# Kernel tuning notes

Measured on AMD Instinct MI355X. Metric: run time of the kernel, lower is better.

## Reference

```python
import jax, jax.numpy as jnp
import numpy as np

S, D_IN, D_OUT = 4096, 1024, 1024

def setup_inputs() -> dict:
    key = jax.random.key(0)
    kx, kq, kk, kv = jax.random.split(key, 4)
    scale = 0.02
    return {
        "x": jax.random.normal(kx, (S, D_IN), dtype=jnp.float32),
        "W_query": jax.random.normal(kq, (D_IN, D_OUT), dtype=jnp.float32) * scale,
        "W_key": jax.random.normal(kk, (D_IN, D_OUT), dtype=jnp.float32) * scale,
        "W_value": jax.random.normal(kv, (D_IN, D_OUT), dtype=jnp.float32) * scale,
    }

def reference(x, W_query, W_key, W_value):
    # x: [S, d_in]; W_*: [d_in, d_out]
    queries = x @ W_query        # [S, d_out]
    keys = x @ W_key             # [S, d_out]
    values = x @ W_value         # [S, d_out]
    d_k = keys.shape[-1]
    attn_scores = queries @ keys.T            # [S, S]
    attn_weights = jax.nn.softmax(attn_scores / jnp.sqrt(jnp.float32(d_k)), axis=-1)
    context_vec = attn_weights @ values       # [S, d_out]
    return context_vec
```

## Files before the change

kernel.cpp:

```cpp
#include <hip/hip_runtime.h>
#include <hip/hip_bf16.h>

typedef _Float16 f16x8 __attribute__((ext_vector_type(8)));
typedef float f32x4 __attribute__((ext_vector_type(4)));
typedef unsigned short u16;
typedef u16 u16x8 __attribute__((ext_vector_type(8)));

__device__ __forceinline__ u16 f2h_bits(float f) {
    _Float16 h = (_Float16)f;
    return __builtin_bit_cast(u16, h);
}
__device__ __forceinline__ float h2f(u16 b) {
    return (float)__builtin_bit_cast(_Float16, b);
}
__device__ __forceinline__ float ld_as_float(const float* p) { return *p; }
__device__ __forceinline__ float ld_as_float(const u16* p)   { return h2f(*p); }

__device__ __forceinline__ void async_ld16(const void* g, void* l) {
    __builtin_amdgcn_global_load_lds(
        (__attribute__((address_space(1))) void*)(void*)g,
        (__attribute__((address_space(3))) void*)l,
        16, 0, 0);
}

__device__ __forceinline__ void store_val(float* p, float v) { *p = v; }
__device__ __forceinline__ void store_val(u16* p, float v)   { *p = f2h_bits(v); }

template <typename OutT>
__global__ __launch_bounds__(256) void gemm_bt(
    const u16* __restrict__ A, int lda,
    const u16* __restrict__ B, int ldb,
    OutT* __restrict__ C, int ldc,
    int Ksplit, float alpha, size_t c_z_stride)
{
    __shared__ __attribute__((aligned(16))) u16 As[128 * 32];
    __shared__ __attribute__((aligned(16))) u16 Bs[128 * 32];

    const int t    = threadIdx.x;
    const int lane = t & 63;
    const int wave = t >> 6;
    const int wm   = wave & 1;
    const int wn   = wave >> 1;
    const int l16  = lane & 15;
    const int quad = lane >> 4;

    const int bm = blockIdx.y;
    const int bn = blockIdx.x;
    const int kz = blockIdx.z;
    A += (size_t)kz * Ksplit;
    B += (size_t)kz * Ksplit;
    C += (size_t)kz * c_z_stride;

    const int srow = t >> 2;
    const int sseg = (t & 3) ^ ((t >> 3) & 3);
    const int scol = sseg * 8;

    const u16* Ag = A + (size_t)(bm * 128 + srow) * lda + scol;
    const u16* Bg = B + (size_t)(bn * 128 + srow) * ldb + scol;
    const size_t a64 = (size_t)64 * lda;
    const size_t b64 = (size_t)64 * ldb;

    u16* AsD0 = &As[t * 8];
    u16* AsD1 = &As[2048 + t * 8];
    u16* BsD0 = &Bs[t * 8];
    u16* BsD1 = &Bs[2048 + t * 8];

    const int fseg = (quad ^ ((l16 >> 1) & 3)) * 8;
    const u16* Afr = &As[(wm * 64 + l16) * 32 + fseg];
    const u16* Bfr = &Bs[(wn * 64 + l16) * 32 + fseg];

    f32x4 acc[4][4] = {};

    for (int k0 = 0; k0 < Ksplit; k0 += 32) {
        async_ld16(Ag + k0,       AsD0);
        async_ld16(Ag + k0 + a64, AsD1);
        async_ld16(Bg + k0,       BsD0);
        async_ld16(Bg + k0 + b64, BsD1);
        __syncthreads();

        f16x8 af[4], bfv[4];
#pragma unroll
        for (int i = 0; i < 4; i++) af[i]  = *(const f16x8*)(Afr + i * 16 * 32);
#pragma unroll
        for (int i = 0; i < 4; i++) bfv[i] = *(const f16x8*)(Bfr + i * 16 * 32);

#pragma unroll
        for (int mi = 0; mi < 4; mi++)
#pragma unroll
            for (int ni = 0; ni < 4; ni++)
                acc[mi][ni] = __builtin_amdgcn_mfma_f32_16x16x32_f16(
                    af[mi], bfv[ni], acc[mi][ni], 0, 0, 0);

        __syncthreads();
    }

    const int crow = bm * 128 + wm * 64 + quad * 4;
    const int ccol = bn * 128 + wn * 64 + l16;
#pragma unroll
    for (int mi = 0; mi < 4; mi++) {
#pragma unroll
        for (int ni = 0; ni < 4; ni++) {
#pragma unroll
            for (int r = 0; r < 4; r++) {
                float v = acc[mi][ni][r] * alpha;
                store_val(C + (size_t)(crow + mi * 16 + r) * ldc + (ccol + ni * 16), v);
            }
        }
    }
}

__global__ __launch_bounds__(256) void cast_to_f16(
    const float* __restrict__ in, u16* __restrict__ out, int n)
{
    int i = (blockIdx.x * 256 + threadIdx.x) * 4;
    if (i + 3 < n) {
        float4 v = *(const float4*)(in + i);
        ushort4 o;
        o.x = f2h_bits(v.x);
        o.y = f2h_bits(v.y);
        o.z = f2h_bits(v.z);
        o.w = f2h_bits(v.w);
        *(ushort4*)(out + i) = o;
    }
}

template <typename InT>
__global__ __launch_bounds__(256) void transpose_to_f16(
    const InT* __restrict__ in, int ld_in,
    u16* __restrict__ out, int ld_out)
{
    __shared__ float tile[32][33];
    const int bx = blockIdx.x * 32;
    const int by = blockIdx.y * 32;
    const int tx = threadIdx.x, ty = threadIdx.y;
#pragma unroll
    for (int j = 0; j < 4; j++)
        tile[ty + j * 8][tx] = ld_as_float(&in[(size_t)(by + ty + j * 8) * ld_in + bx + tx]);
    __syncthreads();
#pragma unroll
    for (int j = 0; j < 4; j++)
        out[(size_t)(bx + ty + j * 8) * ld_out + by + tx] = f2h_bits(tile[tx][ty + j * 8]);
}

__global__ __launch_bounds__(256) void softmax_rows(u16* __restrict__ S)
{
    const int row = blockIdx.x;
    u16* p = S + (size_t)row * 4096 + threadIdx.x * 16;
    const int t = threadIdx.x;

    u16x8 h0 = *(const u16x8*)p;
    u16x8 h1 = *(const u16x8*)(p + 8);
    float v[16];
    float m = -1e30f;
#pragma unroll
    for (int i = 0; i < 8; i++) { v[i]     = h2f(h0[i]); m = fmaxf(m, v[i]); }
#pragma unroll
    for (int i = 0; i < 8; i++) { v[i + 8] = h2f(h1[i]); m = fmaxf(m, v[i + 8]); }
#pragma unroll
    for (int o = 32; o > 0; o >>= 1) m = fmaxf(m, __shfl_xor(m, o));

    __shared__ float redm[4], reds[4];
    if ((t & 63) == 0) redm[t >> 6] = m;
    __syncthreads();
    m = fmaxf(fmaxf(redm[0], redm[1]), fmaxf(redm[2], redm[3]));

    float s = 0.f;
#pragma unroll
    for (int i = 0; i < 16; i++) { v[i] = __expf(v[i] - m); s += v[i]; }
#pragma unroll
    for (int o = 32; o > 0; o >>= 1) s += __shfl_xor(s, o);
    if ((t & 63) == 0) reds[t >> 6] = s;
    __syncthreads();
    s = reds[0] + reds[1] + reds[2] + reds[3];

    const float inv = 1.0f / s;
    u16x8 o0, o1;
#pragma unroll
    for (int i = 0; i < 8; i++) o0[i] = f2h_bits(v[i] * inv);
#pragma unroll
    for (int i = 0; i < 8; i++) o1[i] = f2h_bits(v[i + 8] * inv);
    *(u16x8*)p = o0;
    *(u16x8*)(p + 8) = o1;
}

__global__ __launch_bounds__(256) void add_f32(
    const float* __restrict__ a, const float* __restrict__ b,
    float* __restrict__ o, int n)
{
    int i = (blockIdx.x * 256 + threadIdx.x) * 4;
    if (i + 3 < n) {
        float4 x = *(const float4*)(a + i);
        float4 y = *(const float4*)(b + i);
        float4 z;
        z.x = x.x + y.x; z.y = x.y + y.y; z.z = x.z + y.z; z.w = x.w + y.w;
        *(float4*)(o + i) = z;
    }
}

extern "C" void kernel_launch(void* const* d_in, const int* in_sizes, int n_in,
                              void* d_out, int out_size, void* d_ws, size_t ws_size,
                              hipStream_t stream)
{
    (void)in_sizes; (void)n_in; (void)out_size; (void)ws_size;
    const float* x  = (const float*)d_in[0];
    const float* Wq = (const float*)d_in[1];
    const float* Wk = (const float*)d_in[2];
    const float* Wv = (const float*)d_in[3];
    float* out = (float*)d_out;
    char* ws = (char*)d_ws;

    u16* xb  = (u16*)(ws);
    u16* Wt  = (u16*)(ws + ((size_t)8  << 20));
    u16* QKV = (u16*)(ws + ((size_t)14 << 20));
    u16* Vt  = (u16*)(ws + ((size_t)38 << 20));
    u16* Sb  = (u16*)(ws + ((size_t)46 << 20));
    float* P0 = (float*)ws;
    float* P1 = P0 + (size_t)4096 * 1024;

    const int S = 4096, D = 1024;
    dim3 tb(32, 8);

    cast_to_f16<<<(S * D) / (4 * 256), 256, 0, stream>>>(x, xb, S * D);

    transpose_to_f16<float><<<dim3(32, 32), tb, 0, stream>>>(Wq, D, Wt + 0 * D * D, D);
    transpose_to_f16<float><<<dim3(32, 32), tb, 0, stream>>>(Wk, D, Wt + 1 * D * D, D);
    transpose_to_f16<float><<<dim3(32, 32), tb, 0, stream>>>(Wv, D, Wt + 2 * D * D, D);

    gemm_bt<u16><<<dim3(3072 / 128, S / 128, 1), 256, 0, stream>>>(
        xb, D, Wt, D, QKV, 3072, D, 1.0f, 0);

    transpose_to_f16<u16><<<dim3(D / 32, S / 32), tb, 0, stream>>>(
        QKV + 2048, 3072, Vt, S);

    gemm_bt<u16><<<dim3(S / 128, S / 128, 1), 256, 0, stream>>>(
        QKV + 0, 3072, QKV + 1024, 3072, Sb, S, D, 0.03125f, 0);

    softmax_rows<<<S, 256, 0, stream>>>(Sb);

    gemm_bt<float><<<dim3(D / 128, S / 128, 2), 256, 0, stream>>>(
        Sb, S, Vt, S, P0, D, 2048, 1.0f, (size_t)S * D);

    add_f32<<<(S * D) / (4 * 256), 256, 0, stream>>>(P0, P1, out, S * D);
}
```

Measured before the change: 260.3 us.

## Double GEMM K-tile to 64 and remap blocks to XCDs for L2 locality

The GEMM's shared-memory K tile grows from 32 to 64. This halves the loop iterations and barrier pairs per block and issues eight async loads per thread per step, with an 8-way XOR swizzle to avoid LDS bank conflicts. Block indices are also remapped so each XCD (lin&7) gets a contiguous range of N-columns, aiming to improve L2 reuse of B tiles. The cost is doubled LDS per block (32KB), which may lower occupancy, and the remap assumes grid dimensions divisible by 8·bnDiv.

```diff
diff --git a/kernel.cpp b/kernel.cpp
--- a/kernel.cpp
+++ b/kernel.cpp
@@ -31,10 +31,10 @@
     const u16* __restrict__ A, int lda,
     const u16* __restrict__ B, int ldb,
     OutT* __restrict__ C, int ldc,
-    int Ksplit, float alpha, size_t c_z_stride)
-{
-    __shared__ __attribute__((aligned(16))) u16 As[128 * 32];
-    __shared__ __attribute__((aligned(16))) u16 Bs[128 * 32];
+    int Ksplit, float alpha, size_t c_z_stride, int bnDiv)
+{
+    __shared__ __attribute__((aligned(16))) u16 As[128 * 64];
+    __shared__ __attribute__((aligned(16))) u16 Bs[128 * 64];
 
     const int t    = threadIdx.x;
     const int lane = t & 63;
@@ -44,46 +44,60 @@
     const int l16  = lane & 15;
     const int quad = lane >> 4;
 
-    const int bm = blockIdx.y;
-    const int bn = blockIdx.x;
+    const int lin = blockIdx.y * gridDim.x + blockIdx.x;
+    const int xcd = lin & 7;
+    const int idx = lin >> 3;
+    const int bn  = xcd * bnDiv + idx % bnDiv;
+    const int bm  = idx / bnDiv;
+
     const int kz = blockIdx.z;
     A += (size_t)kz * Ksplit;
     B += (size_t)kz * Ksplit;
     C += (size_t)kz * c_z_stride;
 
-    const int srow = t >> 2;
-    const int sseg = (t & 3) ^ ((t >> 3) & 3);
-    const int scol = sseg * 8;
+    const int srow = t >> 3;
+    const int scol = ((t & 7) ^ ((t >> 3) & 7)) * 8;
 
     const u16* Ag = A + (size_t)(bm * 128 + srow) * lda + scol;
     const u16* Bg = B + (size_t)(bn * 128 + srow) * ldb + scol;
-    const size_t a64 = (size_t)64 * lda;
-    const size_t b64 = (size_t)64 * ldb;
-
-    u16* AsD0 = &As[t * 8];
-    u16* AsD1 = &As[2048 + t * 8];
-    u16* BsD0 = &Bs[t * 8];
-    u16* BsD1 = &Bs[2048 + t * 8];
-
-    const int fseg = (quad ^ ((l16 >> 1) & 3)) * 8;
-    const u16* Afr = &As[(wm * 64 + l16) * 32 + fseg];
-    const u16* Bfr = &Bs[(wn * 64 + l16) * 32 + fseg];
+    const size_t a32 = (size_t)32 * lda;
+    const size_t b32 = (size_t)32 * ldb;
+
+    u16* AsD = &As[t * 8];
+    u16* BsD = &Bs[t * 8];
+
+    const int p0 = (quad ^ (l16 & 7)) * 8;
+    const int p1 = ((quad + 4) ^ (l16 & 7)) * 8;
+    const u16* Afr0 = &As[(wm * 64 + l16) * 64 + p0];
+    const u16* Afr1 = &As[(wm * 64 + l16) * 64 + p1];
+    const u16* Bfr0 = &Bs[(wn * 64 + l16) * 64 + p0];
+    const u16* Bfr1 = &Bs[(wn * 64 + l16) * 64 + p1];
 
     f32x4 acc[4][4] = {};
 
-    for (int k0 = 0; k0 < Ksplit; k0 += 32) {
-        async_ld16(Ag + k0,       AsD0);
-        async_ld16(Ag + k0 + a64, AsD1);
-        async_ld16(Bg + k0,       BsD0);
-        async_ld16(Bg + k0 + b64, BsD1);
+    for (int k0 = 0; k0 < Ksplit; k0 += 64) {
+#pragma unroll
+        for (int r = 0; r < 4; r++) {
+            async_ld16(Ag + k0 + (size_t)r * a32, AsD + r * 2048);
+            async_ld16(Bg + k0 + (size_t)r * b32, BsD + r * 2048);
+        }
         __syncthreads();
 
         f16x8 af[4], bfv[4];
 #pragma unroll
-        for (int i = 0; i < 4; i++) af[i]  = *(const f16x8*)(Afr + i * 16 * 32);
-#pragma unroll
-        for (int i = 0; i < 4; i++) bfv[i] = *(const f16x8*)(Bfr + i * 16 * 32);
-
+        for (int i = 0; i < 4; i++) af[i]  = *(const f16x8*)(Afr0 + i * 1024);
+#pragma unroll
+        for (int i = 0; i < 4; i++) bfv[i] = *(const f16x8*)(Bfr0 + i * 1024);
+#pragma unroll
+        for (int mi = 0; mi < 4; mi++)
+#pragma unroll
+            for (int ni = 0; ni < 4; ni++)
+                acc[mi][ni] = __builtin_amdgcn_mfma_f32_16x16x32_f16(
+                    af[mi], bfv[ni], acc[mi][ni], 0, 0, 0);
+#pragma unroll
+        for (int i = 0; i < 4; i++) af[i]  = *(const f16x8*)(Afr1 + i * 1024);
+#pragma unroll
+        for (int i = 0; i < 4; i++) bfv[i] = *(const f16x8*)(Bfr1 + i * 1024);
 #pragma unroll
         for (int mi = 0; mi < 4; mi++)
 #pragma unroll
@@ -227,18 +241,18 @@
     transpose_to_f16<float><<<dim3(32, 32), tb, 0, stream>>>(Wv, D, Wt + 2 * D * D, D);
 
     gemm_bt<u16><<<dim3(3072 / 128, S / 128, 1), 256, 0, stream>>>(
-        xb, D, Wt, D, QKV, 3072, D, 1.0f, 0);
+        xb, D, Wt, D, QKV, 3072, D, 1.0f, 0, 3);
 
     transpose_to_f16<u16><<<dim3(D / 32, S / 32), tb, 0, stream>>>(
         QKV + 2048, 3072, Vt, S);
 
     gemm_bt<u16><<<dim3(S / 128, S / 128, 1), 256, 0, stream>>>(
-        QKV + 0, 3072, QKV + 1024, 3072, Sb, S, D, 0.03125f, 0);
+        QKV + 0, 3072, QKV + 1024, 3072, Sb, S, D, 0.03125f, 0, 4);
 
     softmax_rows<<<S, 256, 0, stream>>>(Sb);
 
     gemm_bt<float><<<dim3(D / 128, S / 128, 2), 256, 0, stream>>>(
-        Sb, S, Vt, S, P0, D, 2048, 1.0f, (size_t)S * D);
+        Sb, S, Vt, S, P0, D, 2048, 1.0f, (size_t)S * D, 1);
 
     add_f32<<<(S * D) / (4 * 256), 256, 0, stream>>>(P0, P1, out, S * D);
 }
```

Measured after the change: 242.7 us. -6.8%, faster.
